# Performance work log

Hardware: AMD Instinct MI355X
Metric: run time of the kernel (lower is better)

## Reference

```python
import jax, jax.numpy as jnp
import numpy as np

N_EST = 5      # n_estimators
DEPTH = 6      # n_depth
LEAVES = 64    # 2 ** n_depth


def setup_inputs() -> dict:
    key = jax.random.key(0)
    ks = jax.random.split(key, 6)
    N, F, H, L, O = 131072, 256, 384, 64, 16
    X = jax.random.normal(ks[0], (N, F), jnp.float32)
    W1 = jax.random.normal(ks[1], (F, H), jnp.float32) / np.float32(np.sqrt(F))
    b1 = jnp.zeros((H,), jnp.float32)
    W2 = jax.random.normal(ks[2], (H, L), jnp.float32) / np.float32(np.sqrt(H))
    b2 = jnp.zeros((L,), jnp.float32)
    # phi[i] = random choice of n_leaves indices from arange(n_latent) without replacement
    phi = jnp.stack([jax.random.permutation(jax.random.fold_in(ks[3], i), L)[:LEAVES]
                     for i in range(N_EST)]).astype(jnp.int32)  # [E, 64]
    # pi: per-estimator leaf->label distributions (rows on the simplex, as after softmax updates)
    pi = jax.nn.softmax(jax.random.normal(ks[4], (N_EST, LEAVES, O), jnp.float32), axis=-1)
    return {"X": X, "W1": W1, "b1": b1, "W2": W2, "b2": b2, "phi": phi, "pi": pi}


def reference(X, W1, b1, W2, b2, phi, pi):
    # Backbone MLP: sigmoid -> sigmoid, as in keras.Sequential([Dense(h,'sigmoid'), Dense(l,'sigmoid')])
    h = jax.nn.sigmoid(X @ W1 + b1)          # [N, H]
    latent = jax.nn.sigmoid(h @ W2 + b2)     # [N, L]

    N = X.shape[0]
    E = phi.shape[0]
    d = latent[:, phi]                        # gather per estimator -> [N, E, 64]
    decisions = jnp.stack([d, 1.0 - d], axis=-1)  # [N, E, 64, 2] (go-left / go-right probs)

    # Soft tree routing: product of decision probs along each root->leaf path.
    # Level `lev` uses node indices [begin:begin+2**lev); index 0 is unused (matches TF code).
    mu = jnp.ones((N, E, 1, 1), X.dtype)
    begin = 1
    for lev in range(DEPTH):
        end = begin + 2 ** lev
        # reshape [N,E,k,2] -> [N,E,2k,1]; broadcast against [N,E,k_level,2] replaces tile(1,1,2)
        mu = mu.reshape(N, E, -1, 1) * decisions[:, :, begin:end, :]
        begin = end
    mu = mu.reshape(N, E, LEAVES)             # [N, E, 64] leaf arrival probabilities

    # predict: mean over estimators of mu_e @ pi_e
    return jnp.einsum('nel,elo->no', mu, pi) / E
```

## Files before the change

kernel.cpp:

```cpp
#include <hip/hip_runtime.h>
#include <hip/hip_bf16.h>
#include <stdint.h>

#define F_DIM 256
#define H_DIM 384
#define L_DIM 64
#define O_DIM 16
#define E_NUM 5
#define BM 64

#define XK_STRIDE 264
#define H_STRIDE 392
#define LAT_STRIDE 65
#define MU_STRIDE 328

#define LATT_OFF 50176
#define PHIS_OFF 66816
#define SMEM_BYTES 68096

typedef short bf16x8 __attribute__((ext_vector_type(8)));
typedef float f32x4 __attribute__((ext_vector_type(4)));

__device__ __forceinline__ unsigned short f2bf(float f) {
    union { float f; unsigned int u; } v; v.f = f;
    unsigned int u = v.u;
    return (unsigned short)((u + 0x7FFFu + ((u >> 16) & 1u)) >> 16);
}

__device__ __forceinline__ unsigned int pk2(float a, float b) {
#if defined(__has_builtin)
#if __has_builtin(__builtin_amdgcn_cvt_pk_bf16_f32)
    typedef __bf16 bf2 __attribute__((ext_vector_type(2)));
    bf2 p = __builtin_amdgcn_cvt_pk_bf16_f32(a, b);
    union { bf2 v; unsigned int u; } c; c.v = p;
    return c.u;
#else
    return (unsigned int)f2bf(a) | ((unsigned int)f2bf(b) << 16);
#endif
#else
    return (unsigned int)f2bf(a) | ((unsigned int)f2bf(b) << 16);
#endif
}

__device__ __forceinline__ uint2 cvt4(float4 v) {
    uint2 r; r.x = pk2(v.x, v.y); r.y = pk2(v.z, v.w); return r;
}

__device__ __forceinline__ float sigmoidf(float x) {
    return __builtin_amdgcn_rcpf(1.0f + __builtin_amdgcn_exp2f(-1.44269504088896f * x));
}

__global__ void prep_kernel(const float* __restrict__ W1, const float* __restrict__ W2,
                            const float* __restrict__ pi,
                            unsigned short* __restrict__ W1f,
                            unsigned short* __restrict__ W2f,
                            unsigned short* __restrict__ piTf) {
    __shared__ float tile[32][33];
    const int b = blockIdx.x;
    const int tid = threadIdx.x;
    const int tx = tid & 31, ty = tid >> 5;

    if (b < 120) {
        int ks, t0, nks;
        unsigned short* dst;
        if (b < 96) {
            const int fb = b / 12, hb = b % 12;
            #pragma unroll
            for (int s = 0; s < 32; s += 8)
                tile[ty + s][tx] = W1[(size_t)(fb * 32 + ty + s) * H_DIM + hb * 32 + tx];
            ks = fb; t0 = hb * 2; nks = 8; dst = W1f;
        } else {
            const int bb = b - 96, hb = bb / 2, lb = bb % 2;
            #pragma unroll
            for (int s = 0; s < 32; s += 8)
                tile[ty + s][tx] = W2[(size_t)(hb * 32 + ty + s) * L_DIM + lb * 32 + tx];
            ks = hb; t0 = lb * 2; nks = 12; dst = W2f;
        }
        __syncthreads();
        const int t_local = tid >> 7;
        const int r = (tid * 2) & 255;
        const int lane = r >> 2;
        const int e2b = r & 3;
        const int q = lane >> 4, c = lane & 15;
        const int f0 = q * 8 + e2b * 2;
        const int hl = t_local * 16 + c;
        uint2 v;
        v.x = pk2(tile[f0 + 0][hl], tile[f0 + 1][hl]);
        v.y = pk2(tile[f0 + 2][hl], tile[f0 + 3][hl]);
        const size_t off = ((size_t)((t0 + t_local) * nks + ks) * 64 + lane) * 8 + e2b * 2;
        *(uint2*)(dst + off) = v;
    } else {
        for (int i = tid; i < O_DIM * E_NUM * L_DIM; i += 256) {
            const int j = i & 7, lane = (i >> 3) & 63, ks = i >> 9;
            const int q = lane >> 4, c = lane & 15;
            const int k = ks * 32 + q * 8 + j;
            piTf[i] = f2bf(pi[k * O_DIM + c] * 0.2f);
        }
    }
}

__global__ __launch_bounds__(512, 4) void fused_kernel(
    const float* __restrict__ X,
    const unsigned short* __restrict__ W1f,
    const float* __restrict__ b1,
    const unsigned short* __restrict__ W2f,
    const float* __restrict__ b2,
    const int* __restrict__ phi,
    const unsigned short* __restrict__ piTf,
    float* __restrict__ out) {

    __shared__ __align__(16) unsigned char smem[SMEM_BYTES];
    unsigned short* Xs  = (unsigned short*)smem;
    unsigned short* Hs  = (unsigned short*)smem;
    unsigned short* mus = (unsigned short*)smem;
    float*          latT = (float*)(smem + LATT_OFF);
    int*            phis = (int*)(smem + PHIS_OFF);

    if (blockIdx.x < 512 && ((blockIdx.x >> 8) & 1)) {
        __builtin_amdgcn_s_sleep(127);
    }

    const int tid  = threadIdx.x;
    const int wave = tid >> 6;
    const int lane = tid & 63;
    const int q    = lane >> 4;
    const int c    = lane & 15;
    const int row0 = blockIdx.x * BM;

    if (tid < E_NUM * L_DIM) phis[tid] = phi[tid];

    {
        float4 t0[8];
        #pragma unroll
        for (int i = 0; i < 8; ++i)
            t0[i] = *(const float4*)(X + (size_t)(row0 + wave * 8 + i) * F_DIM + lane * 4);
        #pragma unroll
        for (int i = 0; i < 8; ++i)
            *(uint2*)&Xs[(wave * 8 + i) * XK_STRIDE + lane * 4] = cvt4(t0[i]);
    }

    bf16x8 af0[3];
    #pragma unroll
    for (int i = 0; i < 3; ++i)
        af0[i] = *(const bf16x8*)(W1f + ((size_t)((wave * 3 + i) * 8 + 0) * 64 + lane) * 8);

    __syncthreads();

    f32x4 acc[3][4];
    #pragma unroll
    for (int i = 0; i < 3; ++i)
        #pragma unroll
        for (int j = 0; j < 4; ++j)
            acc[i][j] = (f32x4){0.f, 0.f, 0.f, 0.f};

    {
        bf16x8 bf0[4];
        #pragma unroll
        for (int j = 0; j < 4; ++j)
            bf0[j] = *(const bf16x8*)&Xs[(j * 16 + c) * XK_STRIDE + q * 8];
        #pragma unroll
        for (int i = 0; i < 3; ++i)
            #pragma unroll
            for (int j = 0; j < 4; ++j)
                acc[i][j] = __builtin_amdgcn_mfma_f32_16x16x32_bf16(af0[i], bf0[j], acc[i][j], 0, 0, 0);
    }
    #pragma unroll 2
    for (int ks = 1; ks < 8; ++ks) {
        bf16x8 af[3];
        #pragma unroll
        for (int i = 0; i < 3; ++i)
            af[i] = *(const bf16x8*)(W1f + ((size_t)((wave * 3 + i) * 8 + ks) * 64 + lane) * 8);
        bf16x8 bf_[4];
        #pragma unroll
        for (int j = 0; j < 4; ++j)
            bf_[j] = *(const bf16x8*)&Xs[(j * 16 + c) * XK_STRIDE + ks * 32 + q * 8];
        #pragma unroll
        for (int i = 0; i < 3; ++i)
            #pragma unroll
            for (int j = 0; j < 4; ++j)
                acc[i][j] = __builtin_amdgcn_mfma_f32_16x16x32_bf16(af[i], bf_[j], acc[i][j], 0, 0, 0);
    }
    __syncthreads();

    const int lt = wave >> 1;
    bf16x8 wfrag[12];
    #pragma unroll
    for (int ks = 0; ks < 12; ++ks)
        wfrag[ks] = *(const bf16x8*)(W2f + ((size_t)(lt * 12 + ks) * 64 + lane) * 8);

    #pragma unroll
    for (int i = 0; i < 3; ++i) {
        const int n0 = wave * 48 + i * 16 + q * 4;
        float4 bv = *(const float4*)(b1 + n0);
        #pragma unroll
        for (int j = 0; j < 4; ++j) {
            const int m = j * 16 + c;
            uint2 h2;
            h2.x = pk2(sigmoidf(acc[i][j][0] + bv.x), sigmoidf(acc[i][j][1] + bv.y));
            h2.y = pk2(sigmoidf(acc[i][j][2] + bv.z), sigmoidf(acc[i][j][3] + bv.w));
            *(uint2*)&Hs[m * H_STRIDE + n0] = h2;
        }
    }
    __syncthreads();

    {
        const int mbase = (wave & 1) * 2;
        f32x4 acc2[2];
        acc2[0] = (f32x4){0.f, 0.f, 0.f, 0.f};
        acc2[1] = (f32x4){0.f, 0.f, 0.f, 0.f};
        #pragma unroll
        for (int ks = 0; ks < 12; ++ks) {
            #pragma unroll
            for (int j = 0; j < 2; ++j) {
                bf16x8 bf_ = *(const bf16x8*)&Hs[((mbase + j) * 16 + c) * H_STRIDE + ks * 32 + q * 8];
                acc2[j] = __builtin_amdgcn_mfma_f32_16x16x32_bf16(wfrag[ks], bf_, acc2[j], 0, 0, 0);
            }
        }
        const float4 b2v = *(const float4*)(b2 + lt * 16 + q * 4);
        #pragma unroll
        for (int j = 0; j < 2; ++j) {
            const int m = (mbase + j) * 16 + c;
            #pragma unroll
            for (int rg = 0; rg < 4; ++rg) {
                const int l = lt * 16 + q * 4 + rg;
                latT[l * LAT_STRIDE + m] = sigmoidf(acc2[j][rg] + ((const float*)&b2v)[rg]);
            }
        }
    }
    __syncthreads();

    bf16x8 pfrag[10];
    if (wave >= 5) {
        #pragma unroll
        for (int ks = 0; ks < 10; ++ks)
            pfrag[ks] = *(const bf16x8*)(piTf + ((size_t)ks * 64 + lane) * 8);
    }

    if (wave < E_NUM) {
        const int e = wave;
        const int r = lane;
        float mu[64];
        mu[0] = 1.0f;
        #pragma unroll
        for (int lev = 0; lev < 6; ++lev) {
            const int w = 1 << lev;
            #pragma unroll
            for (int i = w - 1; i >= 0; --i) {
                float d = latT[phis[e * 64 + w + i] * LAT_STRIDE + r];
                float m = mu[i];
                mu[2 * i + 1] = m - m * d;
                mu[2 * i]     = m * d;
            }
        }
        #pragma unroll
        for (int j8 = 0; j8 < 8; ++j8) {
            bf16x8 v;
            #pragma unroll
            for (int t = 0; t < 4; ++t) {
                unsigned int p = pk2(mu[j8 * 8 + 2 * t], mu[j8 * 8 + 2 * t + 1]);
                v[2 * t]     = (short)(p & 0xFFFF);
                v[2 * t + 1] = (short)(p >> 16);
            }
            *((bf16x8*)&mus[r * MU_STRIDE + e * 64 + j8 * 8]) = v;
        }
    }
    __syncthreads();

    if (wave >= 5) {
        for (int mt = wave - 5; mt < 4; mt += (wave == 5 ? 3 : 4)) {
            f32x4 acc3 = (f32x4){0.f, 0.f, 0.f, 0.f};
            #pragma unroll
            for (int ks = 0; ks < 10; ++ks) {
                bf16x8 af = *((const bf16x8*)&mus[(mt * 16 + c) * MU_STRIDE + ks * 32 + q * 8]);
                acc3 = __builtin_amdgcn_mfma_f32_16x16x32_bf16(af, pfrag[ks], acc3, 0, 0, 0);
            }
            #pragma unroll
            for (int rg = 0; rg < 4; ++rg) {
                const int m = mt * 16 + q * 4 + rg;
                out[(size_t)(row0 + m) * O_DIM + c] = acc3[rg];
            }
        }
    }
}

extern "C" void kernel_launch(void* const* d_in, const int* in_sizes, int n_in,
                              void* d_out, int out_size, void* d_ws, size_t ws_size,
                              hipStream_t stream) {
    (void)in_sizes; (void)n_in; (void)out_size; (void)ws_size;
    const float* X  = (const float*)d_in[0];
    const float* W1 = (const float*)d_in[1];
    const float* b1 = (const float*)d_in[2];
    const float* W2 = (const float*)d_in[3];
    const float* b2 = (const float*)d_in[4];
    const int*   phi = (const int*)d_in[5];
    const float* pi  = (const float*)d_in[6];
    float* out = (float*)d_out;

    unsigned short* W1f  = (unsigned short*)d_ws;
    unsigned short* W2f  = (unsigned short*)((char*)d_ws + 196608);
    unsigned short* piTf = (unsigned short*)((char*)d_ws + 196608 + 49152);

    prep_kernel<<<121, 256, 0, stream>>>(W1, W2, pi, W1f, W2f, piTf);

    const int nblocks = 131072 / BM;
    fused_kernel<<<nblocks, 512, 0, stream>>>(X, W1f, b1, W2f, b2, phi, piTf, out);
}
```

Before: 240.2 us.

## Prefetch W1 fragments, reassign GEMM2 tiles, fragment-order mu layout, drop sleep

```diff
diff --git a/kernel.cpp b/kernel.cpp
--- a/kernel.cpp
+++ b/kernel.cpp
@@ -12,7 +12,6 @@
 #define XK_STRIDE 264
 #define H_STRIDE 392
 #define LAT_STRIDE 65
-#define MU_STRIDE 328
 
 #define LATT_OFF 50176
 #define PHIS_OFF 66816
@@ -110,15 +109,11 @@
     float* __restrict__ out) {
 
     __shared__ __align__(16) unsigned char smem[SMEM_BYTES];
-    unsigned short* Xs  = (unsigned short*)smem;
-    unsigned short* Hs  = (unsigned short*)smem;
-    unsigned short* mus = (unsigned short*)smem;
+    unsigned short* Xs   = (unsigned short*)smem;
+    unsigned short* Hs   = (unsigned short*)smem;
+    unsigned short* musf = (unsigned short*)smem;
     float*          latT = (float*)(smem + LATT_OFF);
     int*            phis = (int*)(smem + PHIS_OFF);
-
-    if (blockIdx.x < 512 && ((blockIdx.x >> 8) & 1)) {
-        __builtin_amdgcn_s_sleep(127);
-    }
 
     const int tid  = threadIdx.x;
     const int wave = tid >> 6;
@@ -139,10 +134,10 @@
             *(uint2*)&Xs[(wave * 8 + i) * XK_STRIDE + lane * 4] = cvt4(t0[i]);
     }
 
-    bf16x8 af0[3];
+    bf16x8 afA[3];
     #pragma unroll
     for (int i = 0; i < 3; ++i)
-        af0[i] = *(const bf16x8*)(W1f + ((size_t)((wave * 3 + i) * 8 + 0) * 64 + lane) * 8);
+        afA[i] = *(const bf16x8*)(W1f + ((size_t)((wave * 3 + i) * 8 + 0) * 64 + lane) * 8);
 
     __syncthreads();
 
@@ -153,23 +148,14 @@
         for (int j = 0; j < 4; ++j)
             acc[i][j] = (f32x4){0.f, 0.f, 0.f, 0.f};
 
-    {
-        bf16x8 bf0[4];
-        #pragma unroll
-        for (int j = 0; j < 4; ++j)
-            bf0[j] = *(const bf16x8*)&Xs[(j * 16 + c) * XK_STRIDE + q * 8];
-        #pragma unroll
-        for (int i = 0; i < 3; ++i)
-            #pragma unroll
-            for (int j = 0; j < 4; ++j)
-                acc[i][j] = __builtin_amdgcn_mfma_f32_16x16x32_bf16(af0[i], bf0[j], acc[i][j], 0, 0, 0);
-    }
-    #pragma unroll 2
-    for (int ks = 1; ks < 8; ++ks) {
-        bf16x8 af[3];
-        #pragma unroll
-        for (int i = 0; i < 3; ++i)
-            af[i] = *(const bf16x8*)(W1f + ((size_t)((wave * 3 + i) * 8 + ks) * 64 + lane) * 8);
+    #pragma unroll
+    for (int ks = 0; ks < 8; ++ks) {
+        bf16x8 afB[3];
+        if (ks < 7) {
+            #pragma unroll
+            for (int i = 0; i < 3; ++i)
+                afB[i] = *(const bf16x8*)(W1f + ((size_t)((wave * 3 + i) * 8 + ks + 1) * 64 + lane) * 8);
+        }
         bf16x8 bf_[4];
         #pragma unroll
         for (int j = 0; j < 4; ++j)
@@ -178,15 +164,20 @@
         for (int i = 0; i < 3; ++i)
             #pragma unroll
             for (int j = 0; j < 4; ++j)
-                acc[i][j] = __builtin_amdgcn_mfma_f32_16x16x32_bf16(af[i], bf_[j], acc[i][j], 0, 0, 0);
-    }
-    __syncthreads();
-
-    const int lt = wave >> 1;
-    bf16x8 wfrag[12];
+                acc[i][j] = __builtin_amdgcn_mfma_f32_16x16x32_bf16(afA[i], bf_[j], acc[i][j], 0, 0, 0);
+        if (ks < 7) {
+            #pragma unroll
+            for (int i = 0; i < 3; ++i) afA[i] = afB[i];
+        }
+    }
+    __syncthreads();
+
+    const int mt2 = wave >> 1;
+    const int l2b = (wave & 1) * 2;
+    bf16x8 wfrag0[12];
     #pragma unroll
     for (int ks = 0; ks < 12; ++ks)
-        wfrag[ks] = *(const bf16x8*)(W2f + ((size_t)(lt * 12 + ks) * 64 + lane) * 8);
+        wfrag0[ks] = *(const bf16x8*)(W2f + ((size_t)(l2b * 12 + ks) * 64 + lane) * 8);
 
     #pragma unroll
     for (int i = 0; i < 3; ++i) {
@@ -204,26 +195,29 @@
     __syncthreads();
 
     {
-        const int mbase = (wave & 1) * 2;
+        bf16x8 wfrag1[12];
+        #pragma unroll
+        for (int ks = 0; ks < 12; ++ks)
+            wfrag1[ks] = *(const bf16x8*)(W2f + ((size_t)((l2b + 1) * 12 + ks) * 64 + lane) * 8);
+
         f32x4 acc2[2];
         acc2[0] = (f32x4){0.f, 0.f, 0.f, 0.f};
         acc2[1] = (f32x4){0.f, 0.f, 0.f, 0.f};
         #pragma unroll
         for (int ks = 0; ks < 12; ++ks) {
-            #pragma unroll
-            for (int j = 0; j < 2; ++j) {
-                bf16x8 bf_ = *(const bf16x8*)&Hs[((mbase + j) * 16 + c) * H_STRIDE + ks * 32 + q * 8];
-                acc2[j] = __builtin_amdgcn_mfma_f32_16x16x32_bf16(wfrag[ks], bf_, acc2[j], 0, 0, 0);
-            }
-        }
-        const float4 b2v = *(const float4*)(b2 + lt * 16 + q * 4);
-        #pragma unroll
-        for (int j = 0; j < 2; ++j) {
-            const int m = (mbase + j) * 16 + c;
+            bf16x8 bf_ = *(const bf16x8*)&Hs[(mt2 * 16 + c) * H_STRIDE + ks * 32 + q * 8];
+            acc2[0] = __builtin_amdgcn_mfma_f32_16x16x32_bf16(wfrag0[ks], bf_, acc2[0], 0, 0, 0);
+            acc2[1] = __builtin_amdgcn_mfma_f32_16x16x32_bf16(wfrag1[ks], bf_, acc2[1], 0, 0, 0);
+        }
+        #pragma unroll
+        for (int jl = 0; jl < 2; ++jl) {
+            const int lt = l2b + jl;
+            const float4 b2v = *(const float4*)(b2 + lt * 16 + q * 4);
+            const int m = mt2 * 16 + c;
             #pragma unroll
             for (int rg = 0; rg < 4; ++rg) {
                 const int l = lt * 16 + q * 4 + rg;
-                latT[l * LAT_STRIDE + m] = sigmoidf(acc2[j][rg] + ((const float*)&b2v)[rg]);
+                latT[l * LAT_STRIDE + m] = sigmoidf(acc2[jl][rg] + ((const float*)&b2v)[rg]);
             }
         }
     }
@@ -252,6 +246,8 @@
                 mu[2 * i]     = m * d;
             }
         }
+        const int mt = r >> 4;
+        const int rc = r & 15;
         #pragma unroll
         for (int j8 = 0; j8 < 8; ++j8) {
             bf16x8 v;
@@ -261,7 +257,9 @@
                 v[2 * t]     = (short)(p & 0xFFFF);
                 v[2 * t + 1] = (short)(p >> 16);
             }
-            *((bf16x8*)&mus[r * MU_STRIDE + e * 64 + j8 * 8]) = v;
+            const int ksf = 2 * e + (j8 >> 2);
+            const int qf  = j8 & 3;
+            *((bf16x8*)&musf[((mt * 10 + ksf) * 64 + qf * 16 + rc) * 8]) = v;
         }
     }
     __syncthreads();
@@ -271,7 +269,7 @@
             f32x4 acc3 = (f32x4){0.f, 0.f, 0.f, 0.f};
             #pragma unroll
             for (int ks = 0; ks < 10; ++ks) {
-                bf16x8 af = *((const bf16x8*)&mus[(mt * 16 + c) * MU_STRIDE + ks * 32 + q * 8]);
+                bf16x8 af = *((const bf16x8*)&musf[((mt * 10 + ks) * 64 + lane) * 8]);
                 acc3 = __builtin_amdgcn_mfma_f32_16x16x32_bf16(af, pfrag[ks], acc3, 0, 0, 0);
             }
             #pragma unroll
```

Result: slower. 246.1 us (+2.5%).
